# Performance work log

Measured on AMD Instinct MI355X. Metric: run time of the kernel, lower is better.

The kernel has to match this reference:

```python
import jax, jax.numpy as jnp
import numpy as np

BLOCK_SIZE = 64
NUM_SELECTED = 16

def setup_inputs() -> dict:
    key = jax.random.key(0)
    k1, k2 = jax.random.split(key)
    keys = jax.random.normal(k1, (32, 8192, 512), dtype=jnp.float32)
    compression_scores = jax.random.normal(k2, (32, 128), dtype=jnp.float32)
    return {"keys": keys, "compression_scores": compression_scores}

def reference(keys, compression_scores):
    B, S, D = keys.shape
    nb = S // BLOCK_SIZE
    block_scores = compression_scores.reshape(B, nb)
    # top-k block indices per batch (sorted by descending score, like torch.topk)
    _, top_blocks = jax.lax.top_k(block_scores, NUM_SELECTED)  # [B, k]
    # view keys as blocks and gather the selected blocks per batch
    keys_blk = keys.reshape(B, nb, BLOCK_SIZE, D)
    sel = jnp.take_along_axis(keys_blk, top_blocks[:, :, None, None], axis=1)  # [B, k, bs, D]
    return sel.reshape(B, NUM_SELECTED * BLOCK_SIZE, D)
```

## Files before the change

### kernel.cpp

```cpp
#include <hip/hip_runtime.h>


#define NB 128
#define NSEL 16
#define BS 64
#define DIM 512
#define NBATCH 32

__global__ void topk_kernel(const float* __restrict__ scores,
                            int* __restrict__ top) {
    const int b = blockIdx.x;
    const int lane = threadIdx.x;
    float s0 = scores[b * NB + lane];
    float s1 = scores[b * NB + 64 + lane];
    int i0 = lane;
    int i1 = lane + 64;
    #pragma unroll
    for (int it = 0; it < NSEL; ++it) {
        float bv; int bi;
        if (s0 > s1 || (s0 == s1 && i0 < i1)) { bv = s0; bi = i0; }
        else                                  { bv = s1; bi = i1; }
        #pragma unroll
        for (int off = 32; off >= 1; off >>= 1) {
            float ov = __shfl_xor(bv, off);
            int   oi = __shfl_xor(bi, off);
            if (ov > bv || (ov == bv && oi < bi)) { bv = ov; bi = oi; }
        }
        if (lane == 0) top[b * NSEL + it] = bi;
        if (bi == i0) s0 = -INFINITY;
        if (bi == i1) s1 = -INFINITY;
    }
}

__global__ void gather_kernel(const float4* __restrict__ keys,
                              const int* __restrict__ top,
                              float4* __restrict__ out) {
    const int i = blockIdx.x * blockDim.x + threadIdx.x;
    const int col    = i & 127;
    const int row_g  = i >> 7;
    const int within = row_g & 63;
    const int selrow = row_g >> 6;
    const int b      = selrow >> 4;
    const int blk    = top[selrow];
    const int src    = ((b * NB + blk) * BS + within) * 128 + col;
    out[i] = keys[src];
}

extern "C" void kernel_launch(void* const* d_in, const int* in_sizes, int n_in,
                              void* d_out, int out_size, void* d_ws, size_t ws_size,
                              hipStream_t stream) {
    const float* keys   = (const float*)d_in[0];
    const float* scores = (const float*)d_in[1];
    float* out = (float*)d_out;
    int*   top = (int*)d_ws;

    topk_kernel<<<NBATCH, 64, 0, stream>>>(scores, top);

    const int total_f4 = NBATCH * NSEL * BS * (DIM / 4);
    gather_kernel<<<total_f4 / 256, 256, 0, stream>>>(
        (const float4*)keys, top, (float4*)out);
}
```

Baseline: 603.2 us.

## Fuse top-k selection into gather kernel, recomputing block index per workgroup

Removes the separate top-k kernel and its workspace round trip. Each workgroup redundantly runs the wavefront top-k loop up to its own selection index, then copies a quarter of the chosen 64x512 block with strided float4 loads. This saves one kernel launch and the dependent index load. In exchange, every workgroup repeats up to 16 shuffle-reduction rounds, and each of the four wavefronts in a workgroup does this same work.

```diff
diff --git a/kernel.cpp b/kernel.cpp
--- a/kernel.cpp
+++ b/kernel.cpp
@@ -6,17 +6,26 @@
 #define BS 64
 #define DIM 512
 #define NBATCH 32
+#define F4_PER_BLK (BS * DIM / 4)
+#define CHUNKS 4
+#define F4_PER_CHUNK (F4_PER_BLK / CHUNKS)
 
-__global__ void topk_kernel(const float* __restrict__ scores,
-                            int* __restrict__ top) {
-    const int b = blockIdx.x;
-    const int lane = threadIdx.x;
+__global__ __launch_bounds__(256) void
+token_sel_fused(const float4* __restrict__ keys,
+                const float* __restrict__ scores,
+                float4* __restrict__ out) {
+    const int selrow = blockIdx.x >> 2;
+    const int chunk  = blockIdx.x & 3;
+    const int b   = selrow >> 4;
+    const int sel = selrow & 15;
+    const int lane = threadIdx.x & 63;
+
     float s0 = scores[b * NB + lane];
     float s1 = scores[b * NB + 64 + lane];
     int i0 = lane;
     int i1 = lane + 64;
-    #pragma unroll
-    for (int it = 0; it < NSEL; ++it) {
+    int blk = 0;
+    for (int it = 0; it <= sel; ++it) {
         float bv; int bi;
         if (s0 > s1 || (s0 == s1 && i0 < i1)) { bv = s0; bi = i0; }
         else                                  { bv = s1; bi = i1; }
@@ -26,24 +35,20 @@
             int   oi = __shfl_xor(bi, off);
             if (ov > bv || (ov == bv && oi < bi)) { bv = ov; bi = oi; }
         }
-        if (lane == 0) top[b * NSEL + it] = bi;
+        blk = bi;
         if (bi == i0) s0 = -INFINITY;
         if (bi == i1) s1 = -INFINITY;
     }
-}
 
-__global__ void gather_kernel(const float4* __restrict__ keys,
-                              const int* __restrict__ top,
-                              float4* __restrict__ out) {
-    const int i = blockIdx.x * blockDim.x + threadIdx.x;
-    const int col    = i & 127;
-    const int row_g  = i >> 7;
-    const int within = row_g & 63;
-    const int selrow = row_g >> 6;
-    const int b      = selrow >> 4;
-    const int blk    = top[selrow];
-    const int src    = ((b * NB + blk) * BS + within) * 128 + col;
-    out[i] = keys[src];
+    const size_t off4 = (size_t)chunk * F4_PER_CHUNK;
+    const float4* __restrict__ src =
+        keys + (size_t)(b * NB + blk) * F4_PER_BLK + off4;
+    float4* __restrict__ dst =
+        out + (size_t)selrow * F4_PER_BLK + off4;
+    #pragma unroll
+    for (int t = threadIdx.x; t < F4_PER_CHUNK; t += 256) {
+        dst[t] = src[t];
+    }
 }
 
 extern "C" void kernel_launch(void* const* d_in, const int* in_sizes, int n_in,
@@ -52,11 +57,7 @@
     const float* keys   = (const float*)d_in[0];
     const float* scores = (const float*)d_in[1];
     float* out = (float*)d_out;
-    int*   top = (int*)d_ws;
 
-    topk_kernel<<<NBATCH, 64, 0, stream>>>(scores, top);
-
-    const int total_f4 = NBATCH * NSEL * BS * (DIM / 4);
-    gather_kernel<<<total_f4 / 256, 256, 0, stream>>>(
-        (const float4*)keys, top, (float4*)out);
+    token_sel_fused<<<NBATCH * NSEL * CHUNKS, 256, 0, stream>>>(
+        (const float4*)keys, scores, (float4*)out);
 }
```

Result: no change. 602.4 us (-0.1%).
